# Kernel tuning notes

Hardware: AMD Instinct MI355X
Metric: run time of the kernel (lower is better)

Reference implementation:

```python
import jax, jax.numpy as jnp
import numpy as np

E, M, K, INTER = 8, 4096, 2048, 5632
N = 2 * INTER  # gate + up projections fused in w1
TOPK = 2


def setup_inputs() -> dict:
    key = jax.random.key(0)
    k1, k2, k3, k4, k5 = jax.random.split(key, 5)
    a1 = jax.random.normal(k1, (M, K), dtype=jnp.float32)
    w1 = jax.random.normal(k2, (E, N, K), dtype=jnp.float32) * (K ** -0.5)
    w2 = jax.random.normal(k3, (E, K, INTER), dtype=jnp.float32) * (INTER ** -0.5)
    topk_weights = jax.random.uniform(k4, (M, TOPK), dtype=jnp.float32)
    topk_ids = jax.random.randint(k5, (M, TOPK), 0, E, dtype=jnp.int64)
    return {"a1": a1, "w1": w1, "w2": w2,
            "topk_weights": topk_weights, "topk_ids": topk_ids}


def reference(a1, w1, w2, topk_weights, topk_ids):
    # Fused MoE: dispatch (identity/unquantized path) -> per-expert
    # SwiGLU expert GEMMs -> weighted combine over top-k routing.
    n_half = w1.shape[1] // 2
    fused = jnp.zeros((a1.shape[0], topk_ids.shape[1], w2.shape[1]), a1.dtype)  # [M, topk, K]
    for e in range(w1.shape[0]):  # small fixed expert count
        h = jnp.einsum('mk,nk->mn', a1, w1[e])          # [M, N]
        act = jax.nn.silu(h[:, :n_half]) * h[:, n_half:]  # [M, N/2]
        o = jnp.einsum('mn,kn->mk', act, w2[e])          # [M, K]
        mask = (topk_ids == e).astype(a1.dtype)          # [M, topk]
        fused = fused + mask[..., None] * o[:, None, :]
    # combine: weighted reduction over topk -> output [M, K]
    return jnp.einsum('mt,mtk->mk', topk_weights, fused)
```

## Files before the change

### kernel.cpp

```cpp
#include <hip/hip_runtime.h>
#include <hip/hip_bf16.h>

#define NEXP   8
#define MTOK   4096
#define KDIM   2048
#define NINTER 5632
#define NPAIR  8192

#define AS3 __attribute__((address_space(3)))
#define AS1 __attribute__((address_space(1)))

typedef __attribute__((ext_vector_type(4))) float f32x4;
typedef __attribute__((ext_vector_type(8))) short s16x8;

__device__ __forceinline__ short f2bf(float f) {
  union { float f; unsigned u; } v; v.f = f;
  unsigned r = v.u + 0x7FFFu + ((v.u >> 16) & 1u);
  return (short)(r >> 16);
}

__device__ __forceinline__ s16x8 pack8(float4 a, float4 b) {
  s16x8 v;
  v[0] = f2bf(a.x); v[1] = f2bf(a.y); v[2] = f2bf(a.z); v[3] = f2bf(a.w);
  v[4] = f2bf(b.x); v[5] = f2bf(b.y); v[6] = f2bf(b.z); v[7] = f2bf(b.w);
  return v;
}

__global__ __launch_bounds__(256) void cvt_k(const float* __restrict__ src,
                                             unsigned short* __restrict__ dst, size_t n8) {
  size_t i = (size_t)blockIdx.x * blockDim.x + threadIdx.x;
  size_t stride = (size_t)gridDim.x * blockDim.x;
  for (; i < n8; i += stride) {
    const float4* p = (const float4*)(src + i * 8);
    float4 f0 = p[0], f1 = p[1];
    *(s16x8*)(dst + i * 8) = pack8(f0, f1);
  }
}

__global__ __launch_bounds__(512) void route_k(const int* __restrict__ ids,
                                               int* __restrict__ off,
                                               int* __restrict__ list) {
  __shared__ int sids[NPAIR];
  __shared__ int scnt[64][8];
  __shared__ int sstart[64][8];
  __shared__ int s_is64;
  int tid = threadIdx.x;
  if (tid == 0) s_is64 = 1;
  __syncthreads();
  for (int i = tid; i < NPAIR / 2; i += 512)
    if (ids[2 * i + 1] != 0) s_is64 = 0;
  __syncthreads();
  int is64 = s_is64;
  for (int i = tid; i < NPAIR; i += 512) {
    int e = is64 ? ids[2 * i] : ids[i];
    if (e < 0) e = 0; if (e > 7) e = 7;
    sids[i] = e;
  }
  if (tid < 64)
    for (int e = 0; e < 8; ++e) scnt[tid][e] = 0;
  __syncthreads();
  if (tid < 64) {
    int b0 = tid * 128;
    for (int i = 0; i < 128; ++i) ++scnt[tid][sids[b0 + i]];
  }
  __syncthreads();
  if (tid == 0) {
    int tot = 0;
    for (int e = 0; e < 8; ++e) {
      off[e] = tot;
      for (int c = 0; c < 64; ++c) { sstart[c][e] = tot; tot += scnt[c][e]; }
    }
    off[8] = tot;
  }
  __syncthreads();
  if (tid < 64) {
    int b0 = tid * 128;
    for (int i = 0; i < 128; ++i) {
      int p = b0 + i;
      int e = sids[p];
      list[sstart[tid][e]++] = p;
    }
  }
}

template <int BF>
__global__ __launch_bounds__(256, 2) void gemm1_t(const float* __restrict__ a1,
                                                  const unsigned short* __restrict__ a1b,
                                                  const float* __restrict__ w1,
                                                  const unsigned short* __restrict__ w1b,
                                                  const int* __restrict__ off,
                                                  const int* __restrict__ list,
                                                  unsigned short* __restrict__ act) {
  int e = blockIdx.z, mt = blockIdx.y, nt = blockIdx.x;
  int base = off[e];
  int cnt  = off[e + 1] - base;
  if (mt * 128 >= cnt) return;
  __shared__ __align__(16) short lA[128 * 64];
  __shared__ __align__(16) short lBg[128 * 64];
  __shared__ __align__(16) short lBu[128 * 64];
  __shared__ int srow[128];
  int tid = threadIdx.x;
  if (tid < 128) {
    int r = mt * 128 + tid;
    srow[tid] = (r < cnt) ? (list[base + r] >> 1) : 0;
  }
  __syncthreads();
  int lane = tid & 63, wave = tid >> 6;
  int wm = wave >> 1, wn = wave & 1;
  int lrow = lane & 15, lhi = lane >> 4;
  f32x4 accg[4][4], accu[4][4];
#pragma unroll
  for (int i = 0; i < 4; ++i)
#pragma unroll
    for (int j = 0; j < 4; ++j) { accg[i][j] = (f32x4)(0.f); accu[i][j] = (f32x4)(0.f); }
  int n0 = nt * 128;

  const unsigned short* aSrc[4];
  const unsigned short* gSrc[4];
  const unsigned short* uSrc[4];
  if constexpr (BF) {
    const unsigned short* w1be = w1b + (size_t)e * (2 * NINTER) * KDIM;
    int c = lane & 7;
#pragma unroll
    for (int q = 0; q < 4; ++q) {
      int r = wave * 32 + q * 8 + (lane >> 3);
      int swz = (c ^ (r & 7)) * 8;
      aSrc[q] = a1b + (size_t)srow[r] * KDIM + swz;
      gSrc[q] = w1be + (size_t)(n0 + r) * KDIM + swz;
      uSrc[q] = w1be + (size_t)(NINTER + n0 + r) * KDIM + swz;
    }
  }
  const float* w1e = w1 + (size_t)e * (2 * NINTER) * KDIM;

  for (int k0 = 0; k0 < KDIM; k0 += 64) {
    if constexpr (BF) {
#pragma unroll
      for (int q = 0; q < 4; ++q) {
        int row0 = wave * 32 + q * 8;
        __builtin_amdgcn_global_load_lds((const AS1 void*)(aSrc[q] + k0), (AS3 void*)&lA[row0 * 64], 16, 0, 0);
        __builtin_amdgcn_global_load_lds((const AS1 void*)(gSrc[q] + k0), (AS3 void*)&lBg[row0 * 64], 16, 0, 0);
        __builtin_amdgcn_global_load_lds((const AS1 void*)(uSrc[q] + k0), (AS3 void*)&lBu[row0 * 64], 16, 0, 0);
      }
    } else {
#pragma unroll
      for (int c4 = 0; c4 < 4; ++c4) {
        int cid = c4 * 256 + tid;
        int row = cid >> 3, k8 = cid & 7;
        const float* s = a1 + (size_t)srow[row] * KDIM + k0 + k8 * 8;
        float4 f0 = *(const float4*)s;
        float4 f1 = *(const float4*)(s + 4);
        *(s16x8*)&lA[row * 64 + ((k8 ^ (row & 7)) * 8)] = pack8(f0, f1);
      }
#pragma unroll
      for (int c4 = 0; c4 < 4; ++c4) {
        int cid = c4 * 256 + tid;
        int row = cid >> 3, k8 = cid & 7;
        const float* sg = w1e + (size_t)(n0 + row) * KDIM + k0 + k8 * 8;
        const float* su = w1e + (size_t)(NINTER + n0 + row) * KDIM + k0 + k8 * 8;
        float4 g0 = *(const float4*)sg;
        float4 g1 = *(const float4*)(sg + 4);
        float4 u0 = *(const float4*)su;
        float4 u1 = *(const float4*)(su + 4);
        int o = row * 64 + ((k8 ^ (row & 7)) * 8);
        *(s16x8*)&lBg[o] = pack8(g0, g1);
        *(s16x8*)&lBu[o] = pack8(u0, u1);
      }
    }
    __syncthreads();
#pragma unroll
    for (int kk = 0; kk < 2; ++kk) {
      s16x8 af[4], bg[4], bu[4];
      int chunk = kk * 4 + lhi;
#pragma unroll
      for (int i = 0; i < 4; ++i) {
        int r = wm * 64 + i * 16 + lrow;
        af[i] = *(const s16x8*)&lA[r * 64 + ((chunk ^ (r & 7)) * 8)];
      }
#pragma unroll
      for (int j = 0; j < 4; ++j) {
        int r = wn * 64 + j * 16 + lrow;
        int o = r * 64 + ((chunk ^ (r & 7)) * 8);
        bg[j] = *(const s16x8*)&lBg[o];
        bu[j] = *(const s16x8*)&lBu[o];
      }
#pragma unroll
      for (int i = 0; i < 4; ++i)
#pragma unroll
        for (int j = 0; j < 4; ++j) {
          accg[i][j] = __builtin_amdgcn_mfma_f32_16x16x32_bf16(af[i], bg[j], accg[i][j], 0, 0, 0);
          accu[i][j] = __builtin_amdgcn_mfma_f32_16x16x32_bf16(af[i], bu[j], accu[i][j], 0, 0, 0);
        }
    }
    __syncthreads();
  }
#pragma unroll
  for (int i = 0; i < 4; ++i) {
#pragma unroll
    for (int q = 0; q < 4; ++q) {
      int r = wm * 64 + i * 16 + lhi * 4 + q;
      int grow = mt * 128 + r;
      if (grow < cnt) {
        size_t rowoff = (size_t)(base + grow) * NINTER;
#pragma unroll
        for (int j = 0; j < 4; ++j) {
          float g = accg[i][j][q], u = accu[i][j][q];
          float a = (g / (1.f + __expf(-g))) * u;
          int col = n0 + wn * 64 + j * 16 + lrow;
          act[rowoff + col] = (unsigned short)f2bf(a);
        }
      }
    }
  }
}

template <int BF>
__global__ __launch_bounds__(256, 2) void gemm2_t(const unsigned short* __restrict__ act,
                                                  const float* __restrict__ w2,
                                                  const unsigned short* __restrict__ w2b,
                                                  const int* __restrict__ off,
                                                  const int* __restrict__ list,
                                                  const float* __restrict__ tw,
                                                  float* __restrict__ out) {
  int e = blockIdx.z, mt = blockIdx.y, nt = blockIdx.x;
  int base = off[e];
  int cnt  = off[e + 1] - base;
  if (mt * 128 >= cnt) return;
  __shared__ __align__(16) short lA[128 * 64];
  __shared__ __align__(16) short lB[128 * 64];
  int tid = threadIdx.x;
  int lane = tid & 63, wave = tid >> 6;
  int wm = wave >> 1, wn = wave & 1;
  int lrow = lane & 15, lhi = lane >> 4;
  f32x4 acc[4][4];
#pragma unroll
  for (int i = 0; i < 4; ++i)
#pragma unroll
    for (int j = 0; j < 4; ++j) acc[i][j] = (f32x4)(0.f);
  const float* w2e = w2 + (size_t)e * KDIM * NINTER;

  const unsigned short* aSrc[4];
  const unsigned short* bSrc[4];
  if constexpr (BF) {
    const unsigned short* w2be = w2b + (size_t)e * KDIM * NINTER;
    int c = lane & 7;
#pragma unroll
    for (int q = 0; q < 4; ++q) {
      int r = wave * 32 + q * 8 + (lane >> 3);
      int swz = (c ^ (r & 7)) * 8;
      int grow = mt * 128 + r;
      if (grow >= cnt) grow = cnt - 1;
      aSrc[q] = act + (size_t)(base + grow) * NINTER + swz;
      bSrc[q] = w2be + (size_t)(nt * 128 + r) * NINTER + swz;
    }
  }

  for (int k0 = 0; k0 < NINTER; k0 += 64) {
    if constexpr (BF) {
#pragma unroll
      for (int q = 0; q < 4; ++q) {
        int row0 = wave * 32 + q * 8;
        __builtin_amdgcn_global_load_lds((const AS1 void*)(aSrc[q] + k0), (AS3 void*)&lA[row0 * 64], 16, 0, 0);
        __builtin_amdgcn_global_load_lds((const AS1 void*)(bSrc[q] + k0), (AS3 void*)&lB[row0 * 64], 16, 0, 0);
      }
    } else {
#pragma unroll
      for (int c4 = 0; c4 < 4; ++c4) {
        int cid = c4 * 256 + tid;
        int row = cid >> 3, k8 = cid & 7;
        int grow = mt * 128 + row;
        if (grow >= cnt) grow = cnt - 1;
        s16x8 v = *(const s16x8*)(act + (size_t)(base + grow) * NINTER + k0 + k8 * 8);
        *(s16x8*)&lA[row * 64 + ((k8 ^ (row & 7)) * 8)] = v;
      }
#pragma unroll
      for (int c4 = 0; c4 < 4; ++c4) {
        int cid = c4 * 256 + tid;
        int row = cid >> 3, k8 = cid & 7;
        const float* s = w2e + (size_t)(nt * 128 + row) * NINTER + k0 + k8 * 8;
        float4 f0 = *(const float4*)s;
        float4 f1 = *(const float4*)(s + 4);
        *(s16x8*)&lB[row * 64 + ((k8 ^ (row & 7)) * 8)] = pack8(f0, f1);
      }
    }
    __syncthreads();
#pragma unroll
    for (int kk = 0; kk < 2; ++kk) {
      s16x8 af[4], bf[4];
      int chunk = kk * 4 + lhi;
#pragma unroll
      for (int i = 0; i < 4; ++i) {
        int r = wm * 64 + i * 16 + lrow;
        af[i] = *(const s16x8*)&lA[r * 64 + ((chunk ^ (r & 7)) * 8)];
      }
#pragma unroll
      for (int j = 0; j < 4; ++j) {
        int r = wn * 64 + j * 16 + lrow;
        bf[j] = *(const s16x8*)&lB[r * 64 + ((chunk ^ (r & 7)) * 8)];
      }
#pragma unroll
      for (int i = 0; i < 4; ++i)
#pragma unroll
        for (int j = 0; j < 4; ++j)
          acc[i][j] = __builtin_amdgcn_mfma_f32_16x16x32_bf16(af[i], bf[j], acc[i][j], 0, 0, 0);
    }
    __syncthreads();
  }
#pragma unroll
  for (int i = 0; i < 4; ++i) {
#pragma unroll
    for (int q = 0; q < 4; ++q) {
      int r = wm * 64 + i * 16 + lhi * 4 + q;
      int grow = mt * 128 + r;
      if (grow < cnt) {
        int p = list[base + grow];
        int m = p >> 1;
        float wgt = tw[p];
#pragma unroll
        for (int j = 0; j < 4; ++j) {
          int col = nt * 128 + wn * 64 + j * 16 + lrow;
          atomicAdd(&out[(size_t)m * KDIM + col], wgt * acc[i][j][q]);
        }
      }
    }
  }
}

extern "C" void kernel_launch(void* const* d_in, const int* in_sizes, int n_in,
                              void* d_out, int out_size, void* d_ws, size_t ws_size,
                              hipStream_t stream) {
  const float* a1 = (const float*)d_in[0];
  const float* w1 = (const float*)d_in[1];
  const float* w2 = (const float*)d_in[2];
  const float* tw = (const float*)d_in[3];
  const int*   ids = (const int*)d_in[4];
  float* out = (float*)d_out;

  int* off  = (int*)d_ws;
  int* list = off + 16;
  unsigned short* act = (unsigned short*)((char*)d_ws + 65536);
  size_t actB = (size_t)NPAIR * NINTER * 2;
  unsigned short* a1b = (unsigned short*)((char*)act + actB);
  size_t a1B = (size_t)MTOK * KDIM * 2;
  unsigned short* w1b = (unsigned short*)((char*)a1b + a1B);
  size_t w1B = (size_t)NEXP * 2 * NINTER * KDIM * 2;
  unsigned short* w2b = (unsigned short*)((char*)w1b + w1B);
  size_t w2B = (size_t)NEXP * KDIM * NINTER * 2;
  size_t need = 65536 + actB + a1B + w1B + w2B;

  hipMemsetAsync(d_out, 0, (size_t)MTOK * KDIM * sizeof(float), stream);
  route_k<<<1, 512, 0, stream>>>(ids, off, list);

  if (ws_size >= need) {
    cvt_k<<<2048, 256, 0, stream>>>(a1, a1b, a1B / 16);
    cvt_k<<<2048, 256, 0, stream>>>(w1, w1b, w1B / 16);
    cvt_k<<<2048, 256, 0, stream>>>(w2, w2b, w2B / 16);
    gemm1_t<1><<<dim3(NINTER / 128, 64, NEXP), 256, 0, stream>>>(a1, a1b, w1, w1b, off, list, act);
    gemm2_t<1><<<dim3(KDIM / 128, 64, NEXP), 256, 0, stream>>>(act, w2, w2b, off, list, tw, out);
  } else {
    gemm1_t<0><<<dim3(NINTER / 128, 64, NEXP), 256, 0, stream>>>(a1, a1b, w1, w1b, off, list, act);
    gemm2_t<0><<<dim3(KDIM / 128, 64, NEXP), 256, 0, stream>>>(act, w2, w2b, off, list, tw, out);
  }
}
```

Measured before the change: 1.047 ms.

## Double-buffer 256-row MoE GEMM tiles and fold w2 conversion into gemm1

Replaces both expert GEMMs with 512-thread kernels that use 256-row tiles and double-buffered async global-to-LDS loads. They use explicit waitcnt and barrier scheduling plus MFMA priority hints so that loads overlap compute. The separate w2 fp32-to-bf16 conversion kernel is removed; gemm1 blocks each convert a slice of w2 at their start, removing one launch and overlapping that conversion with the GEMM. The larger tiles use about 128KB of dynamic LDS per block, and reordering the conversion depends on every gemm1 block finishing before gemm2 starts.

```diff
diff --git a/kernel.cpp b/kernel.cpp
--- a/kernel.cpp
+++ b/kernel.cpp
@@ -12,6 +12,13 @@
 
 typedef __attribute__((ext_vector_type(4))) float f32x4;
 typedef __attribute__((ext_vector_type(8))) short s16x8;
+
+#define MEMFENCE asm volatile("" ::: "memory")
+#define SB       __builtin_amdgcn_s_barrier()
+#define SCHEDB   __builtin_amdgcn_sched_barrier(0)
+#define WAITV8   asm volatile("s_waitcnt vmcnt(8)" ::: "memory")
+#define WAITV0   asm volatile("s_waitcnt vmcnt(0)" ::: "memory")
+#define WAITLG   asm volatile("s_waitcnt lgkmcnt(0)" ::: "memory")
 
 __device__ __forceinline__ short f2bf(float f) {
   union { float f; unsigned u; } v; v.f = f;
@@ -83,14 +90,300 @@
   }
 }
 
-template <int BF>
-__global__ __launch_bounds__(256, 2) void gemm1_t(const float* __restrict__ a1,
-                                                  const unsigned short* __restrict__ a1b,
-                                                  const float* __restrict__ w1,
-                                                  const unsigned short* __restrict__ w1b,
-                                                  const int* __restrict__ off,
-                                                  const int* __restrict__ list,
-                                                  unsigned short* __restrict__ act) {
+__global__ __launch_bounds__(512, 2) void gemm1_k8(const float* __restrict__ w2f,
+                                                   unsigned short* __restrict__ w2b,
+                                                   const unsigned short* __restrict__ a1b,
+                                                   const unsigned short* __restrict__ w1b,
+                                                   const int* __restrict__ off,
+                                                   const int* __restrict__ list,
+                                                   unsigned short* __restrict__ act) {
+  extern __shared__ __align__(16) char smem[];
+  short* sm = (short*)smem;
+  int* srow = (int*)(sm + 65536);
+
+  int tid = threadIdx.x;
+  {
+    size_t bid = blockIdx.x + (size_t)gridDim.x * (blockIdx.y + (size_t)gridDim.y * blockIdx.z);
+    size_t g = bid * 1024 + tid;
+    if (g < 11534336u) {
+      const float4* s = (const float4*)(w2f + g * 8);
+      float4 f0 = s[0], f1 = s[1];
+      *(s16x8*)(w2b + g * 8) = pack8(f0, f1);
+    }
+    g += 512;
+    if (g < 11534336u) {
+      const float4* s = (const float4*)(w2f + g * 8);
+      float4 f0 = s[0], f1 = s[1];
+      *(s16x8*)(w2b + g * 8) = pack8(f0, f1);
+    }
+  }
+
+  int e = blockIdx.z, mt = blockIdx.y, nt = blockIdx.x;
+  int base = off[e];
+  int cnt  = off[e + 1] - base;
+  if (mt * 256 >= cnt) return;
+
+  for (int i = tid; i < 256; i += 512) {
+    int r = mt * 256 + i;
+    srow[i] = (r < cnt) ? (list[base + r] >> 1) : (list[base + cnt - 1] >> 1);
+  }
+  __syncthreads();
+
+  int lane = tid & 63, w = tid >> 6;
+  int wm = w >> 2, wn = w & 3;
+  int lrow = lane & 15, lhi = lane >> 4;
+  int l8 = lane >> 3, c8 = lane & 7;
+
+  f32x4 accg[8][2], accu[8][2];
+#pragma unroll
+  for (int i = 0; i < 8; ++i)
+#pragma unroll
+    for (int j = 0; j < 2; ++j) { accg[i][j] = (f32x4)(0.f); accu[i][j] = (f32x4)(0.f); }
+
+  const unsigned short* w1be = w1b + (size_t)e * (2 * NINTER) * KDIM;
+  const unsigned short* sA[4];
+  const unsigned short* sG[2];
+  int aD[4], bD[2];
+#pragma unroll
+  for (int q = 0; q < 4; ++q) {
+    int r = q * 64 + w * 8 + l8;
+    sA[q] = a1b + (size_t)srow[r] * KDIM + ((c8 ^ (r & 7)) * 8);
+    aD[q] = (q * 64 + w * 8) * 64;
+  }
+#pragma unroll
+  for (int q = 0; q < 2; ++q) {
+    int r = q * 64 + w * 8 + l8;
+    sG[q] = w1be + (size_t)(nt * 128 + r) * KDIM + ((c8 ^ (r & 7)) * 8);
+    bD[q] = (q * 64 + w * 8) * 64;
+  }
+  const size_t UPOFF = (size_t)NINTER * KDIM;
+
+  auto STAGE = [&](int t, int b) {
+    int ko = t * 64;
+#pragma unroll
+    for (int q = 0; q < 4; ++q)
+      __builtin_amdgcn_global_load_lds((const AS1 void*)(sA[q] + ko), (AS3 void*)(sm + b * 16384 + aD[q]), 16, 0, 0);
+#pragma unroll
+    for (int q = 0; q < 2; ++q) {
+      __builtin_amdgcn_global_load_lds((const AS1 void*)(sG[q] + ko), (AS3 void*)(sm + 32768 + b * 8192 + bD[q]), 16, 0, 0);
+      __builtin_amdgcn_global_load_lds((const AS1 void*)(sG[q] + UPOFF + ko), (AS3 void*)(sm + 49152 + b * 8192 + bD[q]), 16, 0, 0);
+    }
+  };
+
+  STAGE(0, 0);
+  STAGE(1, 1);
+  WAITV8; SCHEDB; MEMFENCE; SB; MEMFENCE; SCHEDB;
+
+  int b = 0;
+  for (int t = 0; t < KDIM / 64; ++t) {
+    s16x8 aL[4][2], bg[2][2], bu[2][2];
+#pragma unroll
+    for (int i = 0; i < 4; ++i)
+#pragma unroll
+      for (int kk = 0; kk < 2; ++kk) {
+        int r = wm * 128 + i * 16 + lrow, ch = kk * 4 + lhi;
+        aL[i][kk] = *(const s16x8*)&sm[b * 16384 + r * 64 + ((ch ^ (r & 7)) * 8)];
+      }
+#pragma unroll
+    for (int j = 0; j < 2; ++j)
+#pragma unroll
+      for (int kk = 0; kk < 2; ++kk) {
+        int r = wn * 32 + j * 16 + lrow, ch = kk * 4 + lhi;
+        bg[j][kk] = *(const s16x8*)&sm[32768 + b * 8192 + r * 64 + ((ch ^ (r & 7)) * 8)];
+        bu[j][kk] = *(const s16x8*)&sm[49152 + b * 8192 + r * 64 + ((ch ^ (r & 7)) * 8)];
+      }
+    __builtin_amdgcn_s_setprio(1);
+#pragma unroll
+    for (int i = 0; i < 4; ++i)
+#pragma unroll
+      for (int j = 0; j < 2; ++j)
+#pragma unroll
+        for (int kk = 0; kk < 2; ++kk) {
+          accg[i][j] = __builtin_amdgcn_mfma_f32_16x16x32_bf16(aL[i][kk], bg[j][kk], accg[i][j], 0, 0, 0);
+          accu[i][j] = __builtin_amdgcn_mfma_f32_16x16x32_bf16(aL[i][kk], bu[j][kk], accu[i][j], 0, 0, 0);
+        }
+    __builtin_amdgcn_s_setprio(0);
+#pragma unroll
+    for (int i = 0; i < 4; ++i)
+#pragma unroll
+      for (int kk = 0; kk < 2; ++kk) {
+        int r = wm * 128 + (i + 4) * 16 + lrow, ch = kk * 4 + lhi;
+        aL[i][kk] = *(const s16x8*)&sm[b * 16384 + r * 64 + ((ch ^ (r & 7)) * 8)];
+      }
+    __builtin_amdgcn_s_setprio(1);
+#pragma unroll
+    for (int i = 0; i < 4; ++i)
+#pragma unroll
+      for (int j = 0; j < 2; ++j)
+#pragma unroll
+        for (int kk = 0; kk < 2; ++kk) {
+          accg[i + 4][j] = __builtin_amdgcn_mfma_f32_16x16x32_bf16(aL[i][kk], bg[j][kk], accg[i + 4][j], 0, 0, 0);
+          accu[i + 4][j] = __builtin_amdgcn_mfma_f32_16x16x32_bf16(aL[i][kk], bu[j][kk], accu[i + 4][j], 0, 0, 0);
+        }
+    __builtin_amdgcn_s_setprio(0);
+
+    WAITLG; SCHEDB; MEMFENCE; SB; MEMFENCE; SCHEDB;
+    if (t + 2 < KDIM / 64) {
+      STAGE(t + 2, b);
+      WAITV8;
+    } else {
+      WAITV0;
+    }
+    SCHEDB; MEMFENCE; SB; MEMFENCE; SCHEDB;
+    b ^= 1;
+  }
+
+#pragma unroll
+  for (int i = 0; i < 8; ++i) {
+#pragma unroll
+    for (int q = 0; q < 4; ++q) {
+      int grow = mt * 256 + wm * 128 + i * 16 + lhi * 4 + q;
+      if (grow < cnt) {
+        size_t rowoff = (size_t)(base + grow) * NINTER;
+#pragma unroll
+        for (int j = 0; j < 2; ++j) {
+          float g = accg[i][j][q], u = accu[i][j][q];
+          float a = (g / (1.f + __expf(-g))) * u;
+          int col = nt * 128 + wn * 32 + j * 16 + lrow;
+          act[rowoff + col] = (unsigned short)f2bf(a);
+        }
+      }
+    }
+  }
+}
+
+__global__ __launch_bounds__(512, 2) void gemm2_k8(const unsigned short* __restrict__ act,
+                                                   const unsigned short* __restrict__ w2b,
+                                                   const int* __restrict__ off,
+                                                   const int* __restrict__ list,
+                                                   const float* __restrict__ tw,
+                                                   float* __restrict__ out) {
+  extern __shared__ __align__(16) char smem[];
+  short* sm = (short*)smem;
+
+  int e = blockIdx.z, mt = blockIdx.y, nt = blockIdx.x;
+  int base = off[e];
+  int cnt  = off[e + 1] - base;
+  if (mt * 256 >= cnt) return;
+
+  int tid = threadIdx.x;
+  int lane = tid & 63, w = tid >> 6;
+  int wm = w >> 2, wn = w & 3;
+  int lrow = lane & 15, lhi = lane >> 4;
+  int l8 = lane >> 3, c8 = lane & 7;
+
+  f32x4 acc[8][4];
+#pragma unroll
+  for (int i = 0; i < 8; ++i)
+#pragma unroll
+    for (int j = 0; j < 4; ++j) acc[i][j] = (f32x4)(0.f);
+
+  const unsigned short* w2be = w2b + (size_t)e * KDIM * NINTER;
+  const unsigned short* sA[4];
+  const unsigned short* sB[4];
+  int dOf[4];
+#pragma unroll
+  for (int q = 0; q < 4; ++q) {
+    int r = q * 64 + w * 8 + l8;
+    int g = mt * 256 + r; if (g >= cnt) g = cnt - 1;
+    int swz = (c8 ^ (r & 7)) * 8;
+    sA[q] = act + (size_t)(base + g) * NINTER + swz;
+    sB[q] = w2be + (size_t)(nt * 256 + r) * NINTER + swz;
+    dOf[q] = (q * 64 + w * 8) * 64;
+  }
+
+  auto STAGE = [&](int t, int b) {
+    int ko = t * 64;
+#pragma unroll
+    for (int q = 0; q < 4; ++q)
+      __builtin_amdgcn_global_load_lds((const AS1 void*)(sA[q] + ko), (AS3 void*)(sm + b * 16384 + dOf[q]), 16, 0, 0);
+#pragma unroll
+    for (int q = 0; q < 4; ++q)
+      __builtin_amdgcn_global_load_lds((const AS1 void*)(sB[q] + ko), (AS3 void*)(sm + 32768 + b * 16384 + dOf[q]), 16, 0, 0);
+  };
+
+  STAGE(0, 0);
+  STAGE(1, 1);
+  WAITV8; SCHEDB; MEMFENCE; SB; MEMFENCE; SCHEDB;
+
+  int b = 0;
+  for (int t = 0; t < NINTER / 64; ++t) {
+    s16x8 aL[4][2], bb[4][2];
+#pragma unroll
+    for (int i = 0; i < 4; ++i)
+#pragma unroll
+      for (int kk = 0; kk < 2; ++kk) {
+        int r = wm * 128 + i * 16 + lrow, ch = kk * 4 + lhi;
+        aL[i][kk] = *(const s16x8*)&sm[b * 16384 + r * 64 + ((ch ^ (r & 7)) * 8)];
+      }
+#pragma unroll
+    for (int j = 0; j < 4; ++j)
+#pragma unroll
+      for (int kk = 0; kk < 2; ++kk) {
+        int r = wn * 64 + j * 16 + lrow, ch = kk * 4 + lhi;
+        bb[j][kk] = *(const s16x8*)&sm[32768 + b * 16384 + r * 64 + ((ch ^ (r & 7)) * 8)];
+      }
+    __builtin_amdgcn_s_setprio(1);
+#pragma unroll
+    for (int i = 0; i < 4; ++i)
+#pragma unroll
+      for (int j = 0; j < 4; ++j)
+#pragma unroll
+        for (int kk = 0; kk < 2; ++kk)
+          acc[i][j] = __builtin_amdgcn_mfma_f32_16x16x32_bf16(aL[i][kk], bb[j][kk], acc[i][j], 0, 0, 0);
+    __builtin_amdgcn_s_setprio(0);
+#pragma unroll
+    for (int i = 0; i < 4; ++i)
+#pragma unroll
+      for (int kk = 0; kk < 2; ++kk) {
+        int r = wm * 128 + (i + 4) * 16 + lrow, ch = kk * 4 + lhi;
+        aL[i][kk] = *(const s16x8*)&sm[b * 16384 + r * 64 + ((ch ^ (r & 7)) * 8)];
+      }
+    __builtin_amdgcn_s_setprio(1);
+#pragma unroll
+    for (int i = 0; i < 4; ++i)
+#pragma unroll
+      for (int j = 0; j < 4; ++j)
+#pragma unroll
+        for (int kk = 0; kk < 2; ++kk)
+          acc[i + 4][j] = __builtin_amdgcn_mfma_f32_16x16x32_bf16(aL[i][kk], bb[j][kk], acc[i + 4][j], 0, 0, 0);
+    __builtin_amdgcn_s_setprio(0);
+
+    WAITLG; SCHEDB; MEMFENCE; SB; MEMFENCE; SCHEDB;
+    if (t + 2 < NINTER / 64) {
+      STAGE(t + 2, b);
+      WAITV8;
+    } else {
+      WAITV0;
+    }
+    SCHEDB; MEMFENCE; SB; MEMFENCE; SCHEDB;
+    b ^= 1;
+  }
+
+#pragma unroll
+  for (int i = 0; i < 8; ++i) {
+#pragma unroll
+    for (int q = 0; q < 4; ++q) {
+      int grow = mt * 256 + wm * 128 + i * 16 + lhi * 4 + q;
+      if (grow < cnt) {
+        int p = list[base + grow];
+        int m = p >> 1;
+        float wgt = tw[p];
+#pragma unroll
+        for (int j = 0; j < 4; ++j) {
+          int col = nt * 256 + wn * 64 + j * 16 + lrow;
+          atomicAdd(&out[(size_t)m * KDIM + col], wgt * acc[i][j][q]);
+        }
+      }
+    }
+  }
+}
+
+__global__ __launch_bounds__(256, 2) void gemm1_fb(const float* __restrict__ a1,
+                                                   const float* __restrict__ w1,
+                                                   const int* __restrict__ off,
+                                                   const int* __restrict__ list,
+                                                   unsigned short* __restrict__ act) {
   int e = blockIdx.z, mt = blockIdx.y, nt = blockIdx.x;
   int base = off[e];
   int cnt  = off[e + 1] - base;
@@ -113,58 +406,31 @@
   for (int i = 0; i < 4; ++i)
 #pragma unroll
     for (int j = 0; j < 4; ++j) { accg[i][j] = (f32x4)(0.f); accu[i][j] = (f32x4)(0.f); }
+  const float* w1e = w1 + (size_t)e * (2 * NINTER) * KDIM;
   int n0 = nt * 128;
-
-  const unsigned short* aSrc[4];
-  const unsigned short* gSrc[4];
-  const unsigned short* uSrc[4];
-  if constexpr (BF) {
-    const unsigned short* w1be = w1b + (size_t)e * (2 * NINTER) * KDIM;
-    int c = lane & 7;
-#pragma unroll
-    for (int q = 0; q < 4; ++q) {
-      int r = wave * 32 + q * 8 + (lane >> 3);
-      int swz = (c ^ (r & 7)) * 8;
-      aSrc[q] = a1b + (size_t)srow[r] * KDIM + swz;
-      gSrc[q] = w1be + (size_t)(n0 + r) * KDIM + swz;
-      uSrc[q] = w1be + (size_t)(NINTER + n0 + r) * KDIM + swz;
-    }
-  }
-  const float* w1e = w1 + (size_t)e * (2 * NINTER) * KDIM;
-
   for (int k0 = 0; k0 < KDIM; k0 += 64) {
-    if constexpr (BF) {
-#pragma unroll
-      for (int q = 0; q < 4; ++q) {
-        int row0 = wave * 32 + q * 8;
-        __builtin_amdgcn_global_load_lds((const AS1 void*)(aSrc[q] + k0), (AS3 void*)&lA[row0 * 64], 16, 0, 0);
-        __builtin_amdgcn_global_load_lds((const AS1 void*)(gSrc[q] + k0), (AS3 void*)&lBg[row0 * 64], 16, 0, 0);
-        __builtin_amdgcn_global_load_lds((const AS1 void*)(uSrc[q] + k0), (AS3 void*)&lBu[row0 * 64], 16, 0, 0);
-      }
-    } else {
-#pragma unroll
-      for (int c4 = 0; c4 < 4; ++c4) {
-        int cid = c4 * 256 + tid;
-        int row = cid >> 3, k8 = cid & 7;
-        const float* s = a1 + (size_t)srow[row] * KDIM + k0 + k8 * 8;
-        float4 f0 = *(const float4*)s;
-        float4 f1 = *(const float4*)(s + 4);
-        *(s16x8*)&lA[row * 64 + ((k8 ^ (row & 7)) * 8)] = pack8(f0, f1);
-      }
-#pragma unroll
-      for (int c4 = 0; c4 < 4; ++c4) {
-        int cid = c4 * 256 + tid;
-        int row = cid >> 3, k8 = cid & 7;
-        const float* sg = w1e + (size_t)(n0 + row) * KDIM + k0 + k8 * 8;
-        const float* su = w1e + (size_t)(NINTER + n0 + row) * KDIM + k0 + k8 * 8;
-        float4 g0 = *(const float4*)sg;
-        float4 g1 = *(const float4*)(sg + 4);
-        float4 u0 = *(const float4*)su;
-        float4 u1 = *(const float4*)(su + 4);
-        int o = row * 64 + ((k8 ^ (row & 7)) * 8);
-        *(s16x8*)&lBg[o] = pack8(g0, g1);
-        *(s16x8*)&lBu[o] = pack8(u0, u1);
-      }
+#pragma unroll
+    for (int c4 = 0; c4 < 4; ++c4) {
+      int cid = c4 * 256 + tid;
+      int row = cid >> 3, k8 = cid & 7;
+      const float* s = a1 + (size_t)srow[row] * KDIM + k0 + k8 * 8;
+      float4 f0 = *(const float4*)s;
+      float4 f1 = *(const float4*)(s + 4);
+      *(s16x8*)&lA[row * 64 + ((k8 ^ (row & 7)) * 8)] = pack8(f0, f1);
+    }
+#pragma unroll
+    for (int c4 = 0; c4 < 4; ++c4) {
+      int cid = c4 * 256 + tid;
+      int row = cid >> 3, k8 = cid & 7;
+      const float* sg = w1e + (size_t)(n0 + row) * KDIM + k0 + k8 * 8;
+      const float* su = w1e + (size_t)(NINTER + n0 + row) * KDIM + k0 + k8 * 8;
+      float4 g0 = *(const float4*)sg;
+      float4 g1 = *(const float4*)(sg + 4);
+      float4 u0 = *(const float4*)su;
+      float4 u1 = *(const float4*)(su + 4);
+      int o = row * 64 + ((k8 ^ (row & 7)) * 8);
+      *(s16x8*)&lBg[o] = pack8(g0, g1);
+      *(s16x8*)&lBu[o] = pack8(u0, u1);
     }
     __syncthreads();
 #pragma unroll
@@ -213,14 +479,12 @@
   }
 }
 
-template <int BF>
-__global__ __launch_bounds__(256, 2) void gemm2_t(const unsigned short* __restrict__ act,
-                                                  const float* __restrict__ w2,
-                                                  const unsigned short* __restrict__ w2b,
-                                                  const int* __restrict__ off,
-                                                  const int* __restrict__ list,
-                                                  const float* __restrict__ tw,
-                                                  float* __restrict__ out) {
+__global__ __launch_bounds__(256, 2) void gemm2_fb(const unsigned short* __restrict__ act,
+                                                   const float* __restrict__ w2,
+                                                   const int* __restrict__ off,
+                                                   const int* __restrict__ list,
+                                                   const float* __restrict__ tw,
+                                                   float* __restrict__ out) {
   int e = blockIdx.z, mt = blockIdx.y, nt = blockIdx.x;
   int base = off[e];
   int cnt  = off[e + 1] - base;
@@ -237,50 +501,24 @@
 #pragma unroll
     for (int j = 0; j < 4; ++j) acc[i][j] = (f32x4)(0.f);
   const float* w2e = w2 + (size_t)e * KDIM * NINTER;
-
-  const unsigned short* aSrc[4];
-  const unsigned short* bSrc[4];
-  if constexpr (BF) {
-    const unsigned short* w2be = w2b + (size_t)e * KDIM * NINTER;
-    int c = lane & 7;
-#pragma unroll
-    for (int q = 0; q < 4; ++q) {
-      int r = wave * 32 + q * 8 + (lane >> 3);
-      int swz = (c ^ (r & 7)) * 8;
-      int grow = mt * 128 + r;
+  for (int k0 = 0; k0 < NINTER; k0 += 64) {
+#pragma unroll
+    for (int c4 = 0; c4 < 4; ++c4) {
+      int cid = c4 * 256 + tid;
+      int row = cid >> 3, k8 = cid & 7;
+      int grow = mt * 128 + row;
       if (grow >= cnt) grow = cnt - 1;
-      aSrc[q] = act + (size_t)(base + grow) * NINTER + swz;
-      bSrc[q] = w2be + (size_t)(nt * 128 + r) * NINTER + swz;
-    }
-  }
-
-  for (int k0 = 0; k0 < NINTER; k0 += 64) {
-    if constexpr (BF) {
-#pragma unroll
-      for (int q = 0; q < 4; ++q) {
-        int row0 = wave * 32 + q * 8;
-        __builtin_amdgcn_global_load_lds((const AS1 void*)(aSrc[q] + k0), (AS3 void*)&lA[row0 * 64], 16, 0, 0);
-        __builtin_amdgcn_global_load_lds((const AS1 void*)(bSrc[q] + k0), (AS3 void*)&lB[row0 * 64], 16, 0, 0);
-      }
-    } else {
-#pragma unroll
-      for (int c4 = 0; c4 < 4; ++c4) {
-        int cid = c4 * 256 + tid;
-        int row = cid >> 3, k8 = cid & 7;
-        int grow = mt * 128 + row;
-        if (grow >= cnt) grow = cnt - 1;
-        s16x8 v = *(const s16x8*)(act + (size_t)(base + grow) * NINTER + k0 + k8 * 8);
-        *(s16x8*)&lA[row * 64 + ((k8 ^ (row & 7)) * 8)] = v;
-      }
-#pragma unroll
-      for (int c4 = 0; c4 < 4; ++c4) {
-        int cid = c4 * 256 + tid;
-        int row = cid >> 3, k8 = cid & 7;
-        const float* s = w2e + (size_t)(nt * 128 + row) * NINTER + k0 + k8 * 8;
-        float4 f0 = *(const float4*)s;
-        float4 f1 = *(const float4*)(s + 4);
-        *(s16x8*)&lB[row * 64 + ((k8 ^ (row & 7)) * 8)] = pack8(f0, f1);
-      }
+      s16x8 v = *(const s16x8*)(act + (size_t)(base + grow) * NINTER + k0 + k8 * 8);
+      *(s16x8*)&lA[row * 64 + ((k8 ^ (row & 7)) * 8)] = v;
+    }
+#pragma unroll
+    for (int c4 = 0; c4 < 4; ++c4) {
+      int cid = c4 * 256 + tid;
+      int row = cid >> 3, k8 = cid & 7;
+      const float* s = w2e + (size_t)(nt * 128 + row) * NINTER + k0 + k8 * 8;
+      float4 f0 = *(const float4*)s;
+      float4 f1 = *(const float4*)(s + 4);
+      *(s16x8*)&lB[row * 64 + ((k8 ^ (row & 7)) * 8)] = pack8(f0, f1);
     }
     __syncthreads();
 #pragma unroll
@@ -351,13 +589,14 @@
   route_k<<<1, 512, 0, stream>>>(ids, off, list);
 
   if (ws_size >= need) {
-    cvt_k<<<2048, 256, 0, stream>>>(a1, a1b, a1B / 16);
-    cvt_k<<<2048, 256, 0, stream>>>(w1, w1b, w1B / 16);
-    cvt_k<<<2048, 256, 0, stream>>>(w2, w2b, w2B / 16);
-    gemm1_t<1><<<dim3(NINTER / 128, 64, NEXP), 256, 0, stream>>>(a1, a1b, w1, w1b, off, list, act);
-    gemm2_t<1><<<dim3(KDIM / 128, 64, NEXP), 256, 0, stream>>>(act, w2, w2b, off, list, tw, out);
+    hipFuncSetAttribute((const void*)gemm1_k8, hipFuncAttributeMaxDynamicSharedMemorySize, 132096);
+    hipFuncSetAttribute((const void*)gemm2_k8, hipFuncAttributeMaxDynamicSharedMemorySize, 131072);
+    cvt_k<<<2048, 256, 0, stream>>>(a1, a1b, (size_t)MTOK * KDIM / 8);
+    cvt_k<<<2048, 256, 0, stream>>>(w1, w1b, (size_t)NEXP * 2 * NINTER * KDIM / 8);
+    gemm1_k8<<<dim3(NINTER / 128, 32, NEXP), 512, 132096, stream>>>(w2, w2b, a1b, w1b, off, list, act);
+    gemm2_k8<<<dim3(KDIM / 256, 32, NEXP), 512, 131072, stream>>>(act, w2b, off, list, tw, out);
   } else {
-    gemm1_t<0><<<dim3(NINTER / 128, 64, NEXP), 256, 0, stream>>>(a1, a1b, w1, w1b, off, list, act);
-    gemm2_t<0><<<dim3(KDIM / 128, 64, NEXP), 256, 0, stream>>>(act, w2, w2b, off, list, tw, out);
-  }
-}
+    gemm1_fb<<<dim3(NINTER / 128, 64, NEXP), 256, 0, stream>>>(a1, w1, off, list, act);
+    gemm2_fb<<<dim3(KDIM / 128, 64, NEXP), 256, 0, stream>>>(act, w2, off, list, tw, out);
+  }
+}
```

Result: slower. 1.187 ms (+13.3%).

## Fold routing into conversion kernel and overlap w2 conversion with gemm1

Applied to the files above, without the earlier changes.

Routing and the a1/w1 bf16 conversion are merged into one kernel, with block 0 doing the routing while the other blocks convert. This removes the serial single-block route launch and two separate conversion launches. The w2 conversion moves into extra gemm1 blocks (grid y grows from 64 to 73), which are scheduled alongside the expert GEMM blocks and so overlap with them. It relies on hand-computed chunk counts (44*9*8 blocks of 3642 elements) covering w2 exactly, and block 0 now carries both routing and conversion work.

```diff
diff --git a/kernel.cpp b/kernel.cpp
--- a/kernel.cpp
+++ b/kernel.cpp
@@ -26,59 +26,70 @@
   return v;
 }
 
-__global__ __launch_bounds__(256) void cvt_k(const float* __restrict__ src,
-                                             unsigned short* __restrict__ dst, size_t n8) {
-  size_t i = (size_t)blockIdx.x * blockDim.x + threadIdx.x;
-  size_t stride = (size_t)gridDim.x * blockDim.x;
-  for (; i < n8; i += stride) {
-    const float4* p = (const float4*)(src + i * 8);
-    float4 f0 = p[0], f1 = p[1];
-    *(s16x8*)(dst + i * 8) = pack8(f0, f1);
-  }
-}
-
-__global__ __launch_bounds__(512) void route_k(const int* __restrict__ ids,
-                                               int* __restrict__ off,
-                                               int* __restrict__ list) {
-  __shared__ int sids[NPAIR];
-  __shared__ int scnt[64][8];
-  __shared__ int sstart[64][8];
-  __shared__ int s_is64;
+#define N8_A1  ((size_t)MTOK * KDIM / 8)
+#define N8_W1  ((size_t)NEXP * 2 * NINTER * KDIM / 8)
+__global__ __launch_bounds__(256) void routecvt_k(const int* __restrict__ ids,
+                                                  int* __restrict__ off,
+                                                  int* __restrict__ list,
+                                                  const float* __restrict__ a1,
+                                                  unsigned short* __restrict__ a1b,
+                                                  const float* __restrict__ w1,
+                                                  unsigned short* __restrict__ w1b) {
   int tid = threadIdx.x;
-  if (tid == 0) s_is64 = 1;
-  __syncthreads();
-  for (int i = tid; i < NPAIR / 2; i += 512)
-    if (ids[2 * i + 1] != 0) s_is64 = 0;
-  __syncthreads();
-  int is64 = s_is64;
-  for (int i = tid; i < NPAIR; i += 512) {
-    int e = is64 ? ids[2 * i] : ids[i];
-    if (e < 0) e = 0; if (e > 7) e = 7;
-    sids[i] = e;
-  }
-  if (tid < 64)
-    for (int e = 0; e < 8; ++e) scnt[tid][e] = 0;
-  __syncthreads();
-  if (tid < 64) {
-    int b0 = tid * 128;
-    for (int i = 0; i < 128; ++i) ++scnt[tid][sids[b0 + i]];
-  }
-  __syncthreads();
-  if (tid == 0) {
-    int tot = 0;
-    for (int e = 0; e < 8; ++e) {
-      off[e] = tot;
-      for (int c = 0; c < 64; ++c) { sstart[c][e] = tot; tot += scnt[c][e]; }
-    }
-    off[8] = tot;
-  }
-  __syncthreads();
-  if (tid < 64) {
-    int b0 = tid * 128;
-    for (int i = 0; i < 128; ++i) {
-      int p = b0 + i;
-      int e = sids[p];
-      list[sstart[tid][e]++] = p;
+  if (blockIdx.x == 0) {
+    __shared__ int sids[NPAIR];
+    __shared__ int scnt[64][8];
+    __shared__ int sstart[64][8];
+    __shared__ int s_is64;
+    if (tid == 0) s_is64 = 1;
+    __syncthreads();
+    for (int i = tid; i < NPAIR / 2; i += 256)
+      if (ids[2 * i + 1] != 0) s_is64 = 0;
+    __syncthreads();
+    int is64 = s_is64;
+    for (int i = tid; i < NPAIR; i += 256) {
+      int e = is64 ? ids[2 * i] : ids[i];
+      if (e < 0) e = 0; if (e > 7) e = 7;
+      sids[i] = e;
+    }
+    if (tid < 64)
+      for (int e = 0; e < 8; ++e) scnt[tid][e] = 0;
+    __syncthreads();
+    if (tid < 64) {
+      int b0 = tid * 128;
+      for (int i = 0; i < 128; ++i) ++scnt[tid][sids[b0 + i]];
+    }
+    __syncthreads();
+    if (tid == 0) {
+      int tot = 0;
+      for (int e = 0; e < 8; ++e) {
+        off[e] = tot;
+        for (int c = 0; c < 64; ++c) { sstart[c][e] = tot; tot += scnt[c][e]; }
+      }
+      off[8] = tot;
+    }
+    __syncthreads();
+    if (tid < 64) {
+      int b0 = tid * 128;
+      for (int i = 0; i < 128; ++i) {
+        int p = b0 + i;
+        int e = sids[p];
+        list[sstart[tid][e]++] = p;
+      }
+    }
+  }
+  size_t i = (size_t)blockIdx.x * 256 + tid;
+  size_t stride = (size_t)gridDim.x * 256;
+  for (; i < N8_A1 + N8_W1; i += stride) {
+    if (i < N8_A1) {
+      const float4* p = (const float4*)(a1 + i * 8);
+      float4 f0 = p[0], f1 = p[1];
+      *(s16x8*)(a1b + i * 8) = pack8(f0, f1);
+    } else {
+      size_t j = i - N8_A1;
+      const float4* p = (const float4*)(w1 + j * 8);
+      float4 f0 = p[0], f1 = p[1];
+      *(s16x8*)(w1b + j * 8) = pack8(f0, f1);
     }
   }
 }
@@ -88,10 +99,30 @@
                                                   const unsigned short* __restrict__ a1b,
                                                   const float* __restrict__ w1,
                                                   const unsigned short* __restrict__ w1b,
+                                                  const float* __restrict__ w2f,
+                                                  unsigned short* __restrict__ w2b,
                                                   const int* __restrict__ off,
                                                   const int* __restrict__ list,
                                                   unsigned short* __restrict__ act) {
   int e = blockIdx.z, mt = blockIdx.y, nt = blockIdx.x;
+  int tid = threadIdx.x;
+
+  if constexpr (BF) {
+    if (mt >= 64) {
+      const size_t N8_W2 = (size_t)NEXP * KDIM * NINTER / 8;
+      size_t ci = (size_t)nt + 44u * ((mt - 64) + 9u * e);
+      size_t g0 = ci * 3642 + tid;
+      size_t end = (ci + 1) * 3642;
+      if (end > N8_W2) end = N8_W2;
+      for (size_t g = g0; g < end; g += 256) {
+        const float4* s = (const float4*)(w2f + g * 8);
+        float4 f0 = s[0], f1 = s[1];
+        *(s16x8*)(w2b + g * 8) = pack8(f0, f1);
+      }
+      return;
+    }
+  }
+
   int base = off[e];
   int cnt  = off[e + 1] - base;
   if (mt * 128 >= cnt) return;
@@ -99,7 +130,6 @@
   __shared__ __align__(16) short lBg[128 * 64];
   __shared__ __align__(16) short lBu[128 * 64];
   __shared__ int srow[128];
-  int tid = threadIdx.x;
   if (tid < 128) {
     int r = mt * 128 + tid;
     srow[tid] = (r < cnt) ? (list[base + r] >> 1) : 0;
@@ -325,6 +355,52 @@
   }
 }
 
+__global__ __launch_bounds__(512) void route_k(const int* __restrict__ ids,
+                                               int* __restrict__ off,
+                                               int* __restrict__ list) {
+  __shared__ int sids[NPAIR];
+  __shared__ int scnt[64][8];
+  __shared__ int sstart[64][8];
+  __shared__ int s_is64;
+  int tid = threadIdx.x;
+  if (tid == 0) s_is64 = 1;
+  __syncthreads();
+  for (int i = tid; i < NPAIR / 2; i += 512)
+    if (ids[2 * i + 1] != 0) s_is64 = 0;
+  __syncthreads();
+  int is64 = s_is64;
+  for (int i = tid; i < NPAIR; i += 512) {
+    int e = is64 ? ids[2 * i] : ids[i];
+    if (e < 0) e = 0; if (e > 7) e = 7;
+    sids[i] = e;
+  }
+  if (tid < 64)
+    for (int e = 0; e < 8; ++e) scnt[tid][e] = 0;
+  __syncthreads();
+  if (tid < 64) {
+    int b0 = tid * 128;
+    for (int i = 0; i < 128; ++i) ++scnt[tid][sids[b0 + i]];
+  }
+  __syncthreads();
+  if (tid == 0) {
+    int tot = 0;
+    for (int e = 0; e < 8; ++e) {
+      off[e] = tot;
+      for (int c = 0; c < 64; ++c) { sstart[c][e] = tot; tot += scnt[c][e]; }
+    }
+    off[8] = tot;
+  }
+  __syncthreads();
+  if (tid < 64) {
+    int b0 = tid * 128;
+    for (int i = 0; i < 128; ++i) {
+      int p = b0 + i;
+      int e = sids[p];
+      list[sstart[tid][e]++] = p;
+    }
+  }
+}
+
 extern "C" void kernel_launch(void* const* d_in, const int* in_sizes, int n_in,
                               void* d_out, int out_size, void* d_ws, size_t ws_size,
                               hipStream_t stream) {
@@ -348,16 +424,14 @@
   size_t need = 65536 + actB + a1B + w1B + w2B;
 
   hipMemsetAsync(d_out, 0, (size_t)MTOK * KDIM * sizeof(float), stream);
-  route_k<<<1, 512, 0, stream>>>(ids, off, list);
 
   if (ws_size >= need) {
-    cvt_k<<<2048, 256, 0, stream>>>(a1, a1b, a1B / 16);
-    cvt_k<<<2048, 256, 0, stream>>>(w1, w1b, w1B / 16);
-    cvt_k<<<2048, 256, 0, stream>>>(w2, w2b, w2B / 16);
-    gemm1_t<1><<<dim3(NINTER / 128, 64, NEXP), 256, 0, stream>>>(a1, a1b, w1, w1b, off, list, act);
+    routecvt_k<<<4096, 256, 0, stream>>>(ids, off, list, a1, a1b, w1, w1b);
+    gemm1_t<1><<<dim3(NINTER / 128, 73, NEXP), 256, 0, stream>>>(a1, a1b, w1, w1b, w2, w2b, off, list, act);
     gemm2_t<1><<<dim3(KDIM / 128, 64, NEXP), 256, 0, stream>>>(act, w2, w2b, off, list, tw, out);
   } else {
-    gemm1_t<0><<<dim3(NINTER / 128, 64, NEXP), 256, 0, stream>>>(a1, a1b, w1, w1b, off, list, act);
+    route_k<<<1, 512, 0, stream>>>(ids, off, list);
+    gemm1_t<0><<<dim3(NINTER / 128, 64, NEXP), 256, 0, stream>>>(a1, a1b, w1, w1b, w2, w2b, off, list, act);
     gemm2_t<0><<<dim3(KDIM / 128, 64, NEXP), 256, 0, stream>>>(act, w2, w2b, off, list, tw, out);
   }
 }
```

After: 1.006 ms. 1.04x faster.
